# Performance work log

Measured on AMD Instinct MI355X. Metric: run time of the kernel, lower is better.

Reference implementation:

```python
import jax, jax.numpy as jnp
import numpy as np

B, N, IN_DIM, OUT_DIM, HEADS = 4, 2048, 128, 32, 8
NEG_SLOPE = 0.2


def setup_inputs() -> dict:
    key = jax.random.key(0)
    k_x, k_adj, k_w, k_as, k_ad = jax.random.split(key, 5)
    x = jax.random.normal(k_x, (B, N, IN_DIM), dtype=jnp.float32)
    adj = jax.random.randint(k_adj, (B, N, N), 0, 2).astype(jnp.float32)
    # xavier_uniform bounds
    lim_w = float(np.sqrt(6.0 / (IN_DIM + OUT_DIM)))
    lim_a = float(np.sqrt(6.0 / (OUT_DIM + 1)))
    W = jax.random.uniform(k_w, (HEADS, IN_DIM, OUT_DIM), dtype=jnp.float32, minval=-lim_w, maxval=lim_w)
    a_src = jax.random.uniform(k_as, (HEADS, OUT_DIM), dtype=jnp.float32, minval=-lim_a, maxval=lim_a)
    a_dst = jax.random.uniform(k_ad, (HEADS, OUT_DIM), dtype=jnp.float32, minval=-lim_a, maxval=lim_a)
    return {"x": x, "adj": adj, "W": W, "a_src": a_src, "a_dst": a_dst}


def reference(x, adj, W, a_src, a_dst):
    # Wh: [B,H,N,O]
    Wh = jnp.einsum('bnf,hfo->bhno', x, W)
    alpha_src = jnp.einsum('bhno,ho->bhn', Wh, a_src)  # [B,H,N]
    alpha_dst = jnp.einsum('bhno,ho->bhn', Wh, a_dst)  # [B,H,N]
    # additive scores e[b,h,i,j] = alpha_src[b,h,i] + alpha_dst[b,h,j]
    e = alpha_src[..., :, None] + alpha_dst[..., None, :]
    e = jnp.where(e >= 0, e, NEG_SLOPE * e)  # leaky_relu(0.2)
    n = adj.shape[-1]
    eye = jnp.eye(n, dtype=adj.dtype)
    mask = (adj + eye[None] > 0)[:, None, :, :]  # [B,1,N,N]
    e = jnp.where(mask, e, -jnp.inf)
    attn = jax.nn.softmax(e, axis=-1)  # every row has self-loop -> finite
    out = jnp.einsum('bhij,bhjo->bhio', attn, Wh)  # [B,H,N,O]
    b = x.shape[0]
    out = jnp.transpose(out, (0, 2, 1, 3)).reshape(b, n, HEADS * OUT_DIM)
    return jax.nn.relu(out)
```

## Files before the change

### kernel.cpp

```cpp
#include <hip/hip_runtime.h>
#include <math.h>

#define BB 4
#define NSZ 2048
#define FDIM 128
#define ODIM 32
#define HH 8

typedef short short8 __attribute__((ext_vector_type(8)));
typedef float f32x4 __attribute__((ext_vector_type(4)));
typedef float f32x2 __attribute__((ext_vector_type(2)));

#define WS_EAP  0
#define WS_EBP  131072
#define WS_ADJB 262144
#define WS_WHF  786432

__device__ __forceinline__ unsigned bfbits(float f) {
    unsigned u = __builtin_bit_cast(unsigned, f);
    return u + 0x7fffu + ((u >> 16) & 1u);
}
__device__ __forceinline__ unsigned bfpack(float a, float b) {
    return __builtin_amdgcn_perm(bfbits(b), bfbits(a), 0x07060302);
}

__global__ __launch_bounds__(256) void k_prep(const float* __restrict__ x,
                                              const float* __restrict__ adj,
                                              const float* __restrict__ W,
                                              const float* __restrict__ a_src,
                                              const float* __restrict__ a_dst,
                                              unsigned* __restrict__ adjb,
                                              int4* __restrict__ whf,
                                              float2* __restrict__ eap,
                                              float* __restrict__ ebe,
                                              float* __restrict__ ebe2) {
    __shared__ float wsl[FDIM * 33];
    __shared__ unsigned short wlds[64][33];
    int t = threadIdx.x;

    if (blockIdx.x < 16384) {
        int g = blockIdx.x * 256 + t;
        int l = g & 7;
        int word = g >> 3;
        int wk = word & 63;
        int row = word >> 6;
        int i = row & (NSZ - 1);
        const float4 v = *(const float4*)&adj[(size_t)row * NSZ + wk * 32 + l * 4];
        unsigned m = 0;
        if (v.x > 0.f) m |= 1u << (l * 4 + 0);
        if (v.y > 0.f) m |= 1u << (l * 4 + 1);
        if (v.z > 0.f) m |= 1u << (l * 4 + 2);
        if (v.w > 0.f) m |= 1u << (l * 4 + 3);
        m |= (unsigned)__shfl_xor((int)m, 1);
        m |= (unsigned)__shfl_xor((int)m, 2);
        m |= (unsigned)__shfl_xor((int)m, 4);
        if (l == 0) {
            int jb = i - wk * 32;
            if (jb >= 0 && jb < 32) m |= 1u << jb;
            adjb[word] = m;
        }
        return;
    }

    int bidx = blockIdx.x - 16384;
    int b = bidx >> 8;
    int h = (bidx >> 5) & 7;
    int nt = bidx & 31;
    int n0 = nt * 64;
    int w = t >> 6, lane = t & 63;
    int col = lane & 15, quad = lane >> 4;

#pragma unroll
    for (int m = 0; m < 16; m++) {
        int idx = t + m * 256;
        wsl[(idx >> 5) * 33 + (idx & 31)] = W[(size_t)h * (FDIM * ODIM) + idx];
    }

    const float* xp = x + ((size_t)(b * NSZ) + n0 + w * 16 + col) * FDIM + quad * 8;
    int4 afr[4];
#pragma unroll
    for (int kt = 0; kt < 4; kt++) {
        float4 xa = *(const float4*)(xp + kt * 32);
        float4 xb = *(const float4*)(xp + kt * 32 + 4);
        afr[kt] = make_int4((int)bfpack(xa.x, xa.y), (int)bfpack(xa.z, xa.w),
                            (int)bfpack(xb.x, xb.y), (int)bfpack(xb.z, xb.w));
    }
    __syncthreads();

    f32x4 alo = {0.f, 0.f, 0.f, 0.f};
    f32x4 ahi = {0.f, 0.f, 0.f, 0.f};
#pragma unroll
    for (int kt = 0; kt < 4; kt++) {
        short8 a8 = __builtin_bit_cast(short8, afr[kt]);
#pragma unroll
        for (int ot = 0; ot < 2; ot++) {
            unsigned d[4];
#pragma unroll
            for (int jp = 0; jp < 4; jp++) {
                float lo = wsl[(kt * 32 + quad * 8 + 2 * jp) * 33 + ot * 16 + col];
                float hi = wsl[(kt * 32 + quad * 8 + 2 * jp + 1) * 33 + ot * 16 + col];
                d[jp] = bfpack(lo, hi);
            }
            int4 bf = make_int4((int)d[0], (int)d[1], (int)d[2], (int)d[3]);
            if (ot == 0)
                alo = __builtin_amdgcn_mfma_f32_16x16x32_bf16(a8,
                        __builtin_bit_cast(short8, bf), alo, 0, 0, 0);
            else
                ahi = __builtin_amdgcn_mfma_f32_16x16x32_bf16(a8,
                        __builtin_bit_cast(short8, bf), ahi, 0, 0, 0);
        }
    }

    float as0 = a_src[h * ODIM + col], as1 = a_src[h * ODIM + 16 + col];
    float ad0 = a_dst[h * ODIM + col], ad1 = a_dst[h * ODIM + 16 + col];
#pragma unroll
    for (int r = 0; r < 4; r++) {
        float pa = alo[r] * as0 + ahi[r] * as1;
        float pb = alo[r] * ad0 + ahi[r] * ad1;
#pragma unroll
        for (int mk = 1; mk <= 8; mk <<= 1) {
            pa += __shfl_xor(pa, mk);
            pb += __shfl_xor(pb, mk);
        }
        if (col == 0) {
            size_t idx = (size_t)(b * HH + h) * NSZ + n0 + w * 16 + quad * 4 + r;
            eap[idx] = make_float2(__expf(pa - 8.f), __expf(0.2f * pa - 8.f));
            ebe[idx]  = __expf(pb - 8.f);
            ebe2[idx] = __expf(0.2f * pb - 8.f);
        }
    }

#pragma unroll
    for (int r = 0; r < 4; r++) {
        wlds[w * 16 + quad * 4 + r][col]      = (unsigned short)(bfbits(alo[r]) >> 16);
        wlds[w * 16 + quad * 4 + r][col + 16] = (unsigned short)(bfbits(ahi[r]) >> 16);
    }
    __syncthreads();
    int jl = w >> 1, ot = w & 1;
    unsigned d[4];
#pragma unroll
    for (int jp = 0; jp < 4; jp++) {
        unsigned lo = wlds[jl * 32 + quad * 8 + 2 * jp][ot * 16 + col];
        unsigned hi = wlds[jl * 32 + quad * 8 + 2 * jp + 1][ot * 16 + col];
        d[jp] = (hi << 16) | lo;
    }
    int fragid = ((b * HH + h) * 64 + nt * 2 + jl) * 2 + ot;
    whf[(size_t)fragid * 64 + lane] = make_int4((int)d[0], (int)d[1], (int)d[2], (int)d[3]);
}

template<int B>
__device__ __forceinline__ unsigned mexp2(unsigned w, unsigned selhi) {
    unsigned lo, hi, r;
    asm("v_bfe_i32 %0, %1, %2, 1" : "=v"(lo) : "v"(w), "i"(B));
    asm("v_bfe_i32 %0, %1, %2, 1" : "=v"(hi) : "v"(w), "i"(B + 1));
    asm("v_bfi_b32 %0, %1, %2, %3" : "=v"(r) : "s"(selhi), "v"(hi), "v"(lo));
    return r;
}

__device__ __forceinline__ int4 pfrag(float eaa, float eab,
                                      f32x4 e0, f32x4 e1, f32x4 g0, f32x4 g1,
                                      unsigned w8, unsigned selhi) {
    f32x2 ea2 = {eaa, eaa}, eb2 = {eab, eab};
    f32x2 p0 = __builtin_elementwise_max(__builtin_shufflevector(e0, e0, 0, 1) * ea2,
                                         __builtin_shufflevector(g0, g0, 0, 1) * eb2);
    f32x2 p1 = __builtin_elementwise_max(__builtin_shufflevector(e0, e0, 2, 3) * ea2,
                                         __builtin_shufflevector(g0, g0, 2, 3) * eb2);
    f32x2 p2 = __builtin_elementwise_max(__builtin_shufflevector(e1, e1, 0, 1) * ea2,
                                         __builtin_shufflevector(g1, g1, 0, 1) * eb2);
    f32x2 p3 = __builtin_elementwise_max(__builtin_shufflevector(e1, e1, 2, 3) * ea2,
                                         __builtin_shufflevector(g1, g1, 2, 3) * eb2);
    unsigned d0, d1, d2, d3;
    asm("v_cvt_pk_bf16_f32 %0, %1, %2" : "=v"(d0) : "v"(p0.x), "v"(p0.y));
    asm("v_cvt_pk_bf16_f32 %0, %1, %2" : "=v"(d1) : "v"(p1.x), "v"(p1.y));
    asm("v_cvt_pk_bf16_f32 %0, %1, %2" : "=v"(d2) : "v"(p2.x), "v"(p2.y));
    asm("v_cvt_pk_bf16_f32 %0, %1, %2" : "=v"(d3) : "v"(p3.x), "v"(p3.y));
    return make_int4((int)(d0 & mexp2<0>(w8, selhi)),
                     (int)(d1 & mexp2<2>(w8, selhi)),
                     (int)(d2 & mexp2<4>(w8, selhi)),
                     (int)(d3 & mexp2<6>(w8, selhi)));
}

__global__ __launch_bounds__(256) void k_gat(const int4* __restrict__ whf,
                                             const float2* __restrict__ eap,
                                             const float* __restrict__ ebe,
                                             const float* __restrict__ ebe2,
                                             const unsigned* __restrict__ adjb,
                                             float* __restrict__ out) {
    __shared__ __align__(16) float smem[4096];
    float* eble = smem;
    float* eblf = smem + 2048;

    int t = threadIdx.x;
    int u = blockIdx.x;
    int unit = (u & 7) * 256 + (u >> 3);
    int b = unit >> 9;
    int h = (unit >> 6) & 7;
    int i0 = (unit & 63) * 32;
    int wave = t >> 6, lane = t & 63;
    int col = lane & 15, quad = lane >> 4, qsh = quad * 8;
    size_t bh = (size_t)(b * HH + h);
    const unsigned selhi = 0xFFFF0000u;

    const float4* ege = (const float4*)(ebe + bh * NSZ);
    const float4* egf = (const float4*)(ebe2 + bh * NSZ);
    ((float4*)eble)[t]       = ege[t];
    ((float4*)eble)[t + 256] = ege[t + 256];
    ((float4*)eblf)[t]       = egf[t];
    ((float4*)eblf)[t + 256] = egf[t + 256];

    float eaa[2], eab[2];
#pragma unroll
    for (int tt = 0; tt < 2; tt++) {
        float2 ev = eap[bh * NSZ + i0 + tt * 16 + col];
        eaa[tt] = ev.x;
        eab[tt] = ev.y;
    }
    const char* mbase = (const char*)(adjb + ((size_t)(b * NSZ) + i0 + col) * 64)
                        + (size_t)wave * 64;
    const int4* bfp = whf + bh * 8192 + (size_t)(wave * 16) * 128 + lane;

    f32x4 acc[2][2], accd[2];
#pragma unroll
    for (int tt = 0; tt < 2; tt++) {
        acc[tt][0] = (f32x4){0.f, 0.f, 0.f, 0.f};
        acc[tt][1] = (f32x4){0.f, 0.f, 0.f, 0.f};
        accd[tt]   = (f32x4){0.f, 0.f, 0.f, 0.f};
    }
    const int4 onesv = make_int4(0x3F803F80, 0x3F803F80, 0x3F803F80, 0x3F803F80);
    short8 bones = __builtin_bit_cast(short8, onesv);

    __syncthreads();

    for (int jt4 = 0; jt4 < 4; jt4++) {
        uint4 m0 = *(const uint4*)(mbase + 0 * 4096 + jt4 * 16);
        uint4 m1 = *(const uint4*)(mbase + 1 * 4096 + jt4 * 16);
        int4 blo[4], bhi[4];
#pragma unroll
        for (int q = 0; q < 4; q++) {
            blo[q] = bfp[(jt4 * 4 + q) * 128];
            bhi[q] = bfp[(jt4 * 4 + q) * 128 + 64];
        }
        unsigned ma[2][4] = {{m0.x, m0.y, m0.z, m0.w},
                             {m1.x, m1.y, m1.z, m1.w}};
#pragma unroll
        for (int q = 0; q < 4; q++) {
            int jt = wave * 16 + jt4 * 4 + q;
            const f32x4* pe = (const f32x4*)&eble[jt * 32 + qsh];
            const f32x4* pf = (const f32x4*)&eblf[jt * 32 + qsh];
            f32x4 e0 = pe[0], e1 = pe[1];
            f32x4 g0 = pf[0], g1 = pf[1];
            short8 b0 = __builtin_bit_cast(short8, blo[q]);
            short8 b1 = __builtin_bit_cast(short8, bhi[q]);
#pragma unroll
            for (int tt = 0; tt < 2; tt++) {
                int4 fr = pfrag(eaa[tt], eab[tt], e0, e1, g0, g1,
                                ma[tt][q] >> qsh, selhi);
                short8 af = __builtin_bit_cast(short8, fr);
                acc[tt][0] = __builtin_amdgcn_mfma_f32_16x16x32_bf16(af, b0, acc[tt][0], 0, 0, 0);
                acc[tt][1] = __builtin_amdgcn_mfma_f32_16x16x32_bf16(af, b1, acc[tt][1], 0, 0, 0);
                accd[tt]   = __builtin_amdgcn_mfma_f32_16x16x32_bf16(af, bones, accd[tt], 0, 0, 0);
            }
        }
    }

    f32x4 (*cb)[3][64] = (f32x4 (*)[3][64])smem;
    __syncthreads();
    if (wave >= 2) {
#pragma unroll
        for (int tt = 0; tt < 2; tt++) {
            int s = (wave - 2) * 2 + tt;
            cb[s][0][lane] = acc[tt][0];
            cb[s][1][lane] = acc[tt][1];
            cb[s][2][lane] = accd[tt];
        }
    }
    __syncthreads();
    if (wave < 2) {
#pragma unroll
        for (int tt = 0; tt < 2; tt++) {
            int s = wave * 2 + tt;
            acc[tt][0] += cb[s][0][lane];
            acc[tt][1] += cb[s][1][lane];
            accd[tt]   += cb[s][2][lane];
        }
    }
    __syncthreads();
    if (wave == 0) {
        cb[0][0][lane] = acc[1][0];
        cb[0][1][lane] = acc[1][1];
        cb[0][2][lane] = accd[1];
    } else if (wave == 1) {
        cb[1][0][lane] = acc[0][0];
        cb[1][1][lane] = acc[0][1];
        cb[1][2][lane] = accd[0];
    }
    __syncthreads();
    if (wave >= 2) return;
    f32x4 A0, A1, AD;
    if (wave == 0) {
        A0 = acc[0][0] + cb[1][0][lane];
        A1 = acc[0][1] + cb[1][1][lane];
        AD = accd[0]   + cb[1][2][lane];
    } else {
        A0 = acc[1][0] + cb[0][0][lane];
        A1 = acc[1][1] + cb[0][1][lane];
        AD = accd[1]   + cb[0][2][lane];
    }

    float* op = out + ((size_t)(b * NSZ) + i0 + wave * 16) * (HH * ODIM) + h * ODIM + col;
#pragma unroll
    for (int r = 0; r < 4; r++) {
        int row = quad * 4 + r;
        float inv = 1.0f / AD[r];
        op[(size_t)row * (HH * ODIM)]      = fmaxf(A0[r] * inv, 0.f);
        op[(size_t)row * (HH * ODIM) + 16] = fmaxf(A1[r] * inv, 0.f);
    }
}

extern "C" void kernel_launch(void* const* d_in, const int* in_sizes, int n_in,
                              void* d_out, int out_size, void* d_ws, size_t ws_size,
                              hipStream_t stream) {
    const float* x     = (const float*)d_in[0];
    const float* adj   = (const float*)d_in[1];
    const float* W     = (const float*)d_in[2];
    const float* a_src = (const float*)d_in[3];
    const float* a_dst = (const float*)d_in[4];
    float* out = (float*)d_out;

    float* ws = (float*)d_ws;
    float2* eap    = (float2*)(ws + WS_EAP);
    float* ebe     = ws + WS_EBP;
    float* ebe2    = ws + WS_EBP + 65536;
    unsigned* adjb = (unsigned*)(ws + WS_ADJB);
    int4* whf      = (int4*)(ws + WS_WHF);

    k_prep<<<dim3(16384 + 1024), dim3(256), 0, stream>>>(x, adj, W, a_src, a_dst,
                                                         adjb, whf, eap, ebe, ebe2);
    k_gat<<<dim3(BB * HH * (NSZ / 32)), dim3(256), 0, stream>>>(whf, eap, ebe, ebe2, adjb, out);
}
```

Measured before the change: 138.1 us.

## Double-buffer mask/Wh loads in GAT loop and batch adjacency packing per block

The main attention loop in k_gat now uses two register buffers, so the adjacency-mask and Wh fragment loads for the next group are issued before the MFMA work on the current group. This is meant to hide global-load latency behind compute. Separately, k_prep reorders its blocks so the Wh-projection blocks come first, and each adjacency-packing block now handles four chunks, cutting that part of the grid from 16384 blocks to 4096. The cost is higher register pressure from the duplicated buffers, which may lower occupancy.

Result: no change. 139.3 us (+0.9%).

```diff
diff --git a/kernel.cpp b/kernel.cpp
--- a/kernel.cpp
+++ b/kernel.cpp
@@ -38,31 +38,35 @@
     __shared__ unsigned short wlds[64][33];
     int t = threadIdx.x;
 
-    if (blockIdx.x < 16384) {
-        int g = blockIdx.x * 256 + t;
-        int l = g & 7;
-        int word = g >> 3;
-        int wk = word & 63;
-        int row = word >> 6;
-        int i = row & (NSZ - 1);
-        const float4 v = *(const float4*)&adj[(size_t)row * NSZ + wk * 32 + l * 4];
-        unsigned m = 0;
-        if (v.x > 0.f) m |= 1u << (l * 4 + 0);
-        if (v.y > 0.f) m |= 1u << (l * 4 + 1);
-        if (v.z > 0.f) m |= 1u << (l * 4 + 2);
-        if (v.w > 0.f) m |= 1u << (l * 4 + 3);
-        m |= (unsigned)__shfl_xor((int)m, 1);
-        m |= (unsigned)__shfl_xor((int)m, 2);
-        m |= (unsigned)__shfl_xor((int)m, 4);
-        if (l == 0) {
-            int jb = i - wk * 32;
-            if (jb >= 0 && jb < 32) m |= 1u << jb;
-            adjb[word] = m;
+    if (blockIdx.x >= 1024) {
+        int bid = blockIdx.x - 1024;
+#pragma unroll
+        for (int it = 0; it < 4; it++) {
+            int g = (it * 4096 + bid) * 256 + t;
+            int l = g & 7;
+            int word = g >> 3;
+            int wk = word & 63;
+            int row = word >> 6;
+            int i = row & (NSZ - 1);
+            const float4 v = *(const float4*)&adj[(size_t)row * NSZ + wk * 32 + l * 4];
+            unsigned m = 0;
+            if (v.x > 0.f) m |= 1u << (l * 4 + 0);
+            if (v.y > 0.f) m |= 1u << (l * 4 + 1);
+            if (v.z > 0.f) m |= 1u << (l * 4 + 2);
+            if (v.w > 0.f) m |= 1u << (l * 4 + 3);
+            m |= (unsigned)__shfl_xor((int)m, 1);
+            m |= (unsigned)__shfl_xor((int)m, 2);
+            m |= (unsigned)__shfl_xor((int)m, 4);
+            if (l == 0) {
+                int jb = i - wk * 32;
+                if (jb >= 0 && jb < 32) m |= 1u << jb;
+                adjb[word] = m;
+            }
         }
         return;
     }
 
-    int bidx = blockIdx.x - 16384;
+    int bidx = blockIdx.x;
     int b = bidx >> 8;
     int h = (bidx >> 5) & 7;
     int nt = bidx & 31;
@@ -229,39 +233,56 @@
     const int4 onesv = make_int4(0x3F803F80, 0x3F803F80, 0x3F803F80, 0x3F803F80);
     short8 bones = __builtin_bit_cast(short8, onesv);
 
-    __syncthreads();
-
-    for (int jt4 = 0; jt4 < 4; jt4++) {
-        uint4 m0 = *(const uint4*)(mbase + 0 * 4096 + jt4 * 16);
-        uint4 m1 = *(const uint4*)(mbase + 1 * 4096 + jt4 * 16);
-        int4 blo[4], bhi[4];
-#pragma unroll
-        for (int q = 0; q < 4; q++) {
-            blo[q] = bfp[(jt4 * 4 + q) * 128];
-            bhi[q] = bfp[(jt4 * 4 + q) * 128 + 64];
-        }
-        unsigned ma[2][4] = {{m0.x, m0.y, m0.z, m0.w},
-                             {m1.x, m1.y, m1.z, m1.w}};
-#pragma unroll
-        for (int q = 0; q < 4; q++) {
-            int jt = wave * 16 + jt4 * 4 + q;
-            const f32x4* pe = (const f32x4*)&eble[jt * 32 + qsh];
-            const f32x4* pf = (const f32x4*)&eblf[jt * 32 + qsh];
-            f32x4 e0 = pe[0], e1 = pe[1];
-            f32x4 g0 = pf[0], g1 = pf[1];
-            short8 b0 = __builtin_bit_cast(short8, blo[q]);
-            short8 b1 = __builtin_bit_cast(short8, bhi[q]);
-#pragma unroll
-            for (int tt = 0; tt < 2; tt++) {
-                int4 fr = pfrag(eaa[tt], eab[tt], e0, e1, g0, g1,
-                                ma[tt][q] >> qsh, selhi);
-                short8 af = __builtin_bit_cast(short8, fr);
-                acc[tt][0] = __builtin_amdgcn_mfma_f32_16x16x32_bf16(af, b0, acc[tt][0], 0, 0, 0);
-                acc[tt][1] = __builtin_amdgcn_mfma_f32_16x16x32_bf16(af, b1, acc[tt][1], 0, 0, 0);
-                accd[tt]   = __builtin_amdgcn_mfma_f32_16x16x32_bf16(af, bones, accd[tt], 0, 0, 0);
-            }
-        }
-    }
+    uint4 m0A, m1A, m0B, m1B;
+    int4 bloA[4], bhiA[4], bloB[4], bhiB[4];
+
+#define LOADG(M0, M1, BLO, BHI, G)                                        \
+    M0 = *(const uint4*)(mbase + 0 * 4096 + (G) * 16);                    \
+    M1 = *(const uint4*)(mbase + 1 * 4096 + (G) * 16);                    \
+    BLO[0] = bfp[((G) * 4 + 0) * 128]; BHI[0] = bfp[((G) * 4 + 0) * 128 + 64]; \
+    BLO[1] = bfp[((G) * 4 + 1) * 128]; BHI[1] = bfp[((G) * 4 + 1) * 128 + 64]; \
+    BLO[2] = bfp[((G) * 4 + 2) * 128]; BHI[2] = bfp[((G) * 4 + 2) * 128 + 64]; \
+    BLO[3] = bfp[((G) * 4 + 3) * 128]; BHI[3] = bfp[((G) * 4 + 3) * 128 + 64];
+
+#define COMPUTE(M0, M1, BLO, BHI, G)                                      \
+    {                                                                     \
+        unsigned ma0[4] = {M0.x, M0.y, M0.z, M0.w};                       \
+        unsigned ma1[4] = {M1.x, M1.y, M1.z, M1.w};                       \
+        _Pragma("unroll")                                                 \
+        for (int q = 0; q < 4; q++) {                                     \
+            int jt = wave * 16 + (G) * 4 + q;                             \
+            const f32x4* pe = (const f32x4*)&eble[jt * 32 + qsh];         \
+            const f32x4* pf = (const f32x4*)&eblf[jt * 32 + qsh];         \
+            f32x4 e0 = pe[0], e1 = pe[1];                                 \
+            f32x4 g0 = pf[0], g1 = pf[1];                                 \
+            short8 b0 = __builtin_bit_cast(short8, BLO[q]);               \
+            short8 b1 = __builtin_bit_cast(short8, BHI[q]);               \
+            _Pragma("unroll")                                             \
+            for (int tt = 0; tt < 2; tt++) {                              \
+                int4 fr = pfrag(eaa[tt], eab[tt], e0, e1, g0, g1,         \
+                                ((tt == 0 ? ma0[q] : ma1[q]) >> qsh), selhi); \
+                short8 af = __builtin_bit_cast(short8, fr);               \
+                acc[tt][0] = __builtin_amdgcn_mfma_f32_16x16x32_bf16(af, b0, acc[tt][0], 0, 0, 0); \
+                acc[tt][1] = __builtin_amdgcn_mfma_f32_16x16x32_bf16(af, b1, acc[tt][1], 0, 0, 0); \
+                accd[tt]   = __builtin_amdgcn_mfma_f32_16x16x32_bf16(af, bones, accd[tt], 0, 0, 0); \
+            }                                                             \
+        }                                                                 \
+    }
+
+    LOADG(m0A, m1A, bloA, bhiA, 0)
+
+    __syncthreads();
+
+    LOADG(m0B, m1B, bloB, bhiB, 1)
+    COMPUTE(m0A, m1A, bloA, bhiA, 0)
+    LOADG(m0A, m1A, bloA, bhiA, 2)
+    COMPUTE(m0B, m1B, bloB, bhiB, 1)
+    LOADG(m0B, m1B, bloB, bhiB, 3)
+    COMPUTE(m0A, m1A, bloA, bhiA, 2)
+    COMPUTE(m0B, m1B, bloB, bhiB, 3)
+
+#undef LOADG
+#undef COMPUTE
 
     f32x4 (*cb)[3][64] = (f32x4 (*)[3][64])smem;
     __syncthreads();
@@ -334,7 +355,7 @@
     unsigned* adjb = (unsigned*)(ws + WS_ADJB);
     int4* whf      = (int4*)(ws + WS_WHF);
 
-    k_prep<<<dim3(16384 + 1024), dim3(256), 0, stream>>>(x, adj, W, a_src, a_dst,
-                                                         adjb, whf, eap, ebe, ebe2);
+    k_prep<<<dim3(1024 + 4096), dim3(256), 0, stream>>>(x, adj, W, a_src, a_dst,
+                                                        adjb, whf, eap, ebe, ebe2);
     k_gat<<<dim3(BB * HH * (NSZ / 32)), dim3(256), 0, stream>>>(whf, eap, ebe, ebe2, adjb, out);
 }
```

## Halve rows per attention block and batch adjacency packing per block

Applied to the files above, without the earlier changes.

The attention kernel now gives each block 16 query rows instead of 32, so each wave runs a single row tile. This doubles the grid to 4096 blocks and reduces the register accumulators per wave. The prep kernel moves the Wh/score blocks to the front of the grid and has each adjacency-packing block handle four chunks, so far fewer blocks are launched. The cost is that every attention block reloads the full column score vectors and Wh fragments for half as much useful work.

Result: no change. 138.1 us (-0.0%).

```diff
diff --git a/kernel.cpp b/kernel.cpp
--- a/kernel.cpp
+++ b/kernel.cpp
@@ -38,31 +38,35 @@
     __shared__ unsigned short wlds[64][33];
     int t = threadIdx.x;
 
-    if (blockIdx.x < 16384) {
-        int g = blockIdx.x * 256 + t;
-        int l = g & 7;
-        int word = g >> 3;
-        int wk = word & 63;
-        int row = word >> 6;
-        int i = row & (NSZ - 1);
-        const float4 v = *(const float4*)&adj[(size_t)row * NSZ + wk * 32 + l * 4];
-        unsigned m = 0;
-        if (v.x > 0.f) m |= 1u << (l * 4 + 0);
-        if (v.y > 0.f) m |= 1u << (l * 4 + 1);
-        if (v.z > 0.f) m |= 1u << (l * 4 + 2);
-        if (v.w > 0.f) m |= 1u << (l * 4 + 3);
-        m |= (unsigned)__shfl_xor((int)m, 1);
-        m |= (unsigned)__shfl_xor((int)m, 2);
-        m |= (unsigned)__shfl_xor((int)m, 4);
-        if (l == 0) {
-            int jb = i - wk * 32;
-            if (jb >= 0 && jb < 32) m |= 1u << jb;
-            adjb[word] = m;
+    if (blockIdx.x >= 1024) {
+        int bid = blockIdx.x - 1024;
+#pragma unroll
+        for (int it = 0; it < 4; it++) {
+            int g = (it * 4096 + bid) * 256 + t;
+            int l = g & 7;
+            int word = g >> 3;
+            int wk = word & 63;
+            int row = word >> 6;
+            int i = row & (NSZ - 1);
+            const float4 v = *(const float4*)&adj[(size_t)row * NSZ + wk * 32 + l * 4];
+            unsigned m = 0;
+            if (v.x > 0.f) m |= 1u << (l * 4 + 0);
+            if (v.y > 0.f) m |= 1u << (l * 4 + 1);
+            if (v.z > 0.f) m |= 1u << (l * 4 + 2);
+            if (v.w > 0.f) m |= 1u << (l * 4 + 3);
+            m |= (unsigned)__shfl_xor((int)m, 1);
+            m |= (unsigned)__shfl_xor((int)m, 2);
+            m |= (unsigned)__shfl_xor((int)m, 4);
+            if (l == 0) {
+                int jb = i - wk * 32;
+                if (jb >= 0 && jb < 32) m |= 1u << jb;
+                adjb[word] = m;
+            }
         }
         return;
     }
 
-    int bidx = blockIdx.x - 16384;
+    int bidx = blockIdx.x;
     int b = bidx >> 8;
     int h = (bidx >> 5) & 7;
     int nt = bidx & 31;
@@ -192,10 +196,10 @@
 
     int t = threadIdx.x;
     int u = blockIdx.x;
-    int unit = (u & 7) * 256 + (u >> 3);
-    int b = unit >> 9;
-    int h = (unit >> 6) & 7;
-    int i0 = (unit & 63) * 32;
+    int unit = (u & 7) * 512 + (u >> 3);
+    int b = unit >> 10;
+    int h = (unit >> 7) & 7;
+    int i0 = (unit & 127) * 16;
     int wave = t >> 6, lane = t & 63;
     int col = lane & 15, quad = lane >> 4, qsh = quad * 8;
     size_t bh = (size_t)(b * HH + h);
@@ -208,112 +212,78 @@
     ((float4*)eblf)[t]       = egf[t];
     ((float4*)eblf)[t + 256] = egf[t + 256];
 
-    float eaa[2], eab[2];
-#pragma unroll
-    for (int tt = 0; tt < 2; tt++) {
-        float2 ev = eap[bh * NSZ + i0 + tt * 16 + col];
-        eaa[tt] = ev.x;
-        eab[tt] = ev.y;
-    }
+    float2 ev = eap[bh * NSZ + i0 + col];
+    float eaa = ev.x, eab = ev.y;
     const char* mbase = (const char*)(adjb + ((size_t)(b * NSZ) + i0 + col) * 64)
                         + (size_t)wave * 64;
     const int4* bfp = whf + bh * 8192 + (size_t)(wave * 16) * 128 + lane;
 
-    f32x4 acc[2][2], accd[2];
-#pragma unroll
-    for (int tt = 0; tt < 2; tt++) {
-        acc[tt][0] = (f32x4){0.f, 0.f, 0.f, 0.f};
-        acc[tt][1] = (f32x4){0.f, 0.f, 0.f, 0.f};
-        accd[tt]   = (f32x4){0.f, 0.f, 0.f, 0.f};
-    }
+    f32x4 a0 = {0.f, 0.f, 0.f, 0.f};
+    f32x4 a1 = {0.f, 0.f, 0.f, 0.f};
+    f32x4 ad = {0.f, 0.f, 0.f, 0.f};
     const int4 onesv = make_int4(0x3F803F80, 0x3F803F80, 0x3F803F80, 0x3F803F80);
     short8 bones = __builtin_bit_cast(short8, onesv);
 
     __syncthreads();
 
-    for (int jt4 = 0; jt4 < 4; jt4++) {
-        uint4 m0 = *(const uint4*)(mbase + 0 * 4096 + jt4 * 16);
-        uint4 m1 = *(const uint4*)(mbase + 1 * 4096 + jt4 * 16);
+    for (int g = 0; g < 4; g++) {
+        uint4 m0 = *(const uint4*)(mbase + g * 16);
         int4 blo[4], bhi[4];
 #pragma unroll
         for (int q = 0; q < 4; q++) {
-            blo[q] = bfp[(jt4 * 4 + q) * 128];
-            bhi[q] = bfp[(jt4 * 4 + q) * 128 + 64];
-        }
-        unsigned ma[2][4] = {{m0.x, m0.y, m0.z, m0.w},
-                             {m1.x, m1.y, m1.z, m1.w}};
+            blo[q] = bfp[(g * 4 + q) * 128];
+            bhi[q] = bfp[(g * 4 + q) * 128 + 64];
+        }
+        unsigned ma[4] = {m0.x, m0.y, m0.z, m0.w};
 #pragma unroll
         for (int q = 0; q < 4; q++) {
-            int jt = wave * 16 + jt4 * 4 + q;
+            int jt = wave * 16 + g * 4 + q;
             const f32x4* pe = (const f32x4*)&eble[jt * 32 + qsh];
             const f32x4* pf = (const f32x4*)&eblf[jt * 32 + qsh];
             f32x4 e0 = pe[0], e1 = pe[1];
             f32x4 g0 = pf[0], g1 = pf[1];
+            int4 fr = pfrag(eaa, eab, e0, e1, g0, g1, ma[q] >> qsh, selhi);
+            short8 af = __builtin_bit_cast(short8, fr);
             short8 b0 = __builtin_bit_cast(short8, blo[q]);
             short8 b1 = __builtin_bit_cast(short8, bhi[q]);
-#pragma unroll
-            for (int tt = 0; tt < 2; tt++) {
-                int4 fr = pfrag(eaa[tt], eab[tt], e0, e1, g0, g1,
-                                ma[tt][q] >> qsh, selhi);
-                short8 af = __builtin_bit_cast(short8, fr);
-                acc[tt][0] = __builtin_amdgcn_mfma_f32_16x16x32_bf16(af, b0, acc[tt][0], 0, 0, 0);
-                acc[tt][1] = __builtin_amdgcn_mfma_f32_16x16x32_bf16(af, b1, acc[tt][1], 0, 0, 0);
-                accd[tt]   = __builtin_amdgcn_mfma_f32_16x16x32_bf16(af, bones, accd[tt], 0, 0, 0);
-            }
+            a0 = __builtin_amdgcn_mfma_f32_16x16x32_bf16(af, b0, a0, 0, 0, 0);
+            a1 = __builtin_amdgcn_mfma_f32_16x16x32_bf16(af, b1, a1, 0, 0, 0);
+            ad = __builtin_amdgcn_mfma_f32_16x16x32_bf16(af, bones, ad, 0, 0, 0);
         }
     }
 
     f32x4 (*cb)[3][64] = (f32x4 (*)[3][64])smem;
     __syncthreads();
     if (wave >= 2) {
-#pragma unroll
-        for (int tt = 0; tt < 2; tt++) {
-            int s = (wave - 2) * 2 + tt;
-            cb[s][0][lane] = acc[tt][0];
-            cb[s][1][lane] = acc[tt][1];
-            cb[s][2][lane] = accd[tt];
-        }
+        cb[wave - 2][0][lane] = a0;
+        cb[wave - 2][1][lane] = a1;
+        cb[wave - 2][2][lane] = ad;
     }
     __syncthreads();
     if (wave < 2) {
-#pragma unroll
-        for (int tt = 0; tt < 2; tt++) {
-            int s = wave * 2 + tt;
-            acc[tt][0] += cb[s][0][lane];
-            acc[tt][1] += cb[s][1][lane];
-            accd[tt]   += cb[s][2][lane];
-        }
-    }
-    __syncthreads();
-    if (wave == 0) {
-        cb[0][0][lane] = acc[1][0];
-        cb[0][1][lane] = acc[1][1];
-        cb[0][2][lane] = accd[1];
-    } else if (wave == 1) {
-        cb[1][0][lane] = acc[0][0];
-        cb[1][1][lane] = acc[0][1];
-        cb[1][2][lane] = accd[0];
-    }
-    __syncthreads();
-    if (wave >= 2) return;
-    f32x4 A0, A1, AD;
-    if (wave == 0) {
-        A0 = acc[0][0] + cb[1][0][lane];
-        A1 = acc[0][1] + cb[1][1][lane];
-        AD = accd[0]   + cb[1][2][lane];
-    } else {
-        A0 = acc[1][0] + cb[0][0][lane];
-        A1 = acc[1][1] + cb[0][1][lane];
-        AD = accd[1]   + cb[0][2][lane];
-    }
-
-    float* op = out + ((size_t)(b * NSZ) + i0 + wave * 16) * (HH * ODIM) + h * ODIM + col;
+        a0 += cb[wave][0][lane];
+        a1 += cb[wave][1][lane];
+        ad += cb[wave][2][lane];
+    }
+    __syncthreads();
+    if (wave == 1) {
+        cb[0][0][lane] = a0;
+        cb[0][1][lane] = a1;
+        cb[0][2][lane] = ad;
+    }
+    __syncthreads();
+    if (wave != 0) return;
+    a0 += cb[0][0][lane];
+    a1 += cb[0][1][lane];
+    ad += cb[0][2][lane];
+
+    float* op = out + ((size_t)(b * NSZ) + i0) * (HH * ODIM) + h * ODIM + col;
 #pragma unroll
     for (int r = 0; r < 4; r++) {
         int row = quad * 4 + r;
-        float inv = 1.0f / AD[r];
-        op[(size_t)row * (HH * ODIM)]      = fmaxf(A0[r] * inv, 0.f);
-        op[(size_t)row * (HH * ODIM) + 16] = fmaxf(A1[r] * inv, 0.f);
+        float inv = 1.0f / ad[r];
+        op[(size_t)row * (HH * ODIM)]      = fmaxf(a0[r] * inv, 0.f);
+        op[(size_t)row * (HH * ODIM) + 16] = fmaxf(a1[r] * inv, 0.f);
     }
 }
 
@@ -334,7 +304,7 @@
     unsigned* adjb = (unsigned*)(ws + WS_ADJB);
     int4* whf      = (int4*)(ws + WS_WHF);
 
-    k_prep<<<dim3(16384 + 1024), dim3(256), 0, stream>>>(x, adj, W, a_src, a_dst,
-                                                         adjb, whf, eap, ebe, ebe2);
-    k_gat<<<dim3(BB * HH * (NSZ / 32)), dim3(256), 0, stream>>>(whf, eap, ebe, ebe2, adjb, out);
-}
+    k_prep<<<dim3(1024 + 4096), dim3(256), 0, stream>>>(x, adj, W, a_src, a_dst,
+                                                        adjb, whf, eap, ebe, ebe2);
+    k_gat<<<dim3(BB * HH * (NSZ / 16)), dim3(256), 0, stream>>>(whf, eap, ebe, ebe2, adjb, out);
+}
```
